# Optimization experiments

Hardware: AMD Instinct MI355X
Metric: run time of the kernel (lower is better)

The kernel has to match this reference:

```python
import jax, jax.numpy as jnp
import numpy as np

DIM = 256
HEADS = 8
HEAD_DIM = DIM // HEADS
EPS = 1e-5


def layer_norm(x, g, b):
    mu = jnp.mean(x, axis=-1, keepdims=True)
    var = jnp.mean(jnp.square(x - mu), axis=-1, keepdims=True)
    return (x - mu) * jax.lax.rsqrt(var + EPS) * g + b


def setup_inputs() -> dict:
    key = jax.random.key(0)
    ks = jax.random.split(key, 10)
    s = 0.02
    return {
        "x": jax.random.normal(ks[0], (4, DIM, 64, 64), dtype=jnp.float32),
        "g1": jnp.ones((DIM,), jnp.float32),
        "b1": jnp.zeros((DIM,), jnp.float32),
        "Wqkv": jax.random.normal(ks[1], (DIM, 3 * DIM), jnp.float32) * s,
        "Wp": jax.random.normal(ks[2], (DIM, DIM), jnp.float32) * s,
        "bp": jnp.zeros((DIM,), jnp.float32),
        "g2": jnp.ones((DIM,), jnp.float32),
        "b2": jnp.zeros((DIM,), jnp.float32),
        "W1": jax.random.normal(ks[3], (DIM, 2 * DIM), jnp.float32) * s,
        "bf1": jnp.zeros((2 * DIM,), jnp.float32),
        "W2": jax.random.normal(ks[4], (2 * DIM, DIM), jnp.float32) * s,
        "bf2": jnp.zeros((DIM,), jnp.float32),
    }


def reference(x, g1, b1, Wqkv, Wp, bp, g2, b2, W1, bf1, W2, bf2):
    B, C, H, W = x.shape
    N = H * W
    scale = HEAD_DIM ** -0.5
    tokens = x.reshape(B, C, N).transpose(0, 2, 1)  # [B,N,C]
    t = layer_norm(tokens, g1, b1)
    qkv = (t @ Wqkv).reshape(B, N, 3, HEADS, HEAD_DIM)
    q = qkv[:, :, 0].transpose(0, 2, 1, 3)  # [B,h,N,d]
    k = qkv[:, :, 1].transpose(0, 2, 1, 3)
    v = qkv[:, :, 2].transpose(0, 2, 1, 3)
    attn = jax.nn.softmax(jnp.einsum("bhnd,bhmd->bhnm", q, k) * scale, axis=-1)
    out = jnp.einsum("bhnm,bhmd->bhnd", attn, v)
    out = out.transpose(0, 2, 1, 3).reshape(B, N, C)
    tokens = tokens + out @ Wp + bp
    t2 = layer_norm(tokens, g2, b2)
    h = jax.nn.gelu(t2 @ W1 + bf1, approximate=False)
    tokens = tokens + h @ W2 + bf2
    return tokens.transpose(0, 2, 1).reshape(B, C, H, W)
```

## Files before the change

### kernel.cpp

```cpp
#include <hip/hip_runtime.h>

typedef unsigned short u16;
typedef unsigned int   u32;

using bf16x8 = __attribute__((ext_vector_type(8))) __bf16;
using f32x4  = __attribute__((ext_vector_type(4))) float;
using f32x16 = __attribute__((ext_vector_type(16))) float;

#define MFMA16(a, b, c) __builtin_amdgcn_mfma_f32_16x16x32_bf16((a), (b), (c), 0, 0, 0)
#define MFMA32(a, b, c) __builtin_amdgcn_mfma_f32_32x32x16_bf16((a), (b), (c), 0, 0, 0)

__device__ inline u16 f2bf(float f) {
  u32 x = __float_as_uint(f);
  return (u16)((x + 0x7FFFu + ((x >> 16) & 1u)) >> 16);
}

__device__ inline const bf16x8* bfp(const u16* p) {
  return reinterpret_cast<const bf16x8*>(p);
}

__global__ __launch_bounds__(256) void k_conv(
    const float* __restrict__ Wqkv, const float* __restrict__ Wp,
    const float* __restrict__ W1,   const float* __restrict__ W2,
    u16* __restrict__ wqkvT, u16* __restrict__ wpT,
    u16* __restrict__ w1T,   u16* __restrict__ w2T) {
  __shared__ float tile[32][33];
  int blk = blockIdx.x;
  const float* src; u16* dst; int R, C, t;
  if (blk < 192)      { src = Wqkv; dst = wqkvT; R = 256; C = 768; t = blk; }
  else if (blk < 256) { src = Wp;   dst = wpT;   R = 256; C = 256; t = blk - 192; }
  else if (blk < 384) { src = W1;   dst = w1T;   R = 256; C = 512; t = blk - 256; }
  else                { src = W2;   dst = w2T;   R = 512; C = 256; t = blk - 384; }
  int tpc = C >> 5;
  int tr = (t / tpc) << 5, tc = (t % tpc) << 5;
  int j = threadIdx.x & 31, iq = threadIdx.x >> 5;
  #pragma unroll
  for (int i = 0; i < 4; ++i)
    tile[iq + 8 * i][j] = src[(size_t)(tr + iq + 8 * i) * C + tc + j];
  __syncthreads();
  #pragma unroll
  for (int i = 0; i < 4; ++i)
    dst[(size_t)(tc + iq + 8 * i) * R + tr + j] = f2bf(tile[j][iq + 8 * i]);
}

__global__ __launch_bounds__(256) void k_ln1(
    const float* __restrict__ x, const float* __restrict__ g1,
    const float* __restrict__ b1, float* __restrict__ tokens,
    u16* __restrict__ ln) {
  __shared__ float tile[256][33];
  __shared__ float red[2][8][32];
  __shared__ float stat[2][32];
  int tid = threadIdx.x;
  int blk = blockIdx.x;
  int b = blk >> 7, n0 = (blk & 127) << 5;
  {
    int cq = tid >> 5, j = tid & 31;
    const float* xp = x + (((size_t)b * 256) << 12) + n0 + j;
    #pragma unroll 8
    for (int it = 0; it < 32; ++it) {
      int c = it * 8 + cq;
      tile[c][j] = xp[(size_t)c << 12];
    }
  }
  __syncthreads();
  {
    int tn = tid & 31, qq = tid >> 5;
    float s = 0.f, s2 = 0.f;
    #pragma unroll 8
    for (int i = 0; i < 32; ++i) {
      float v = tile[qq * 32 + i][tn];
      s += v; s2 += v * v;
    }
    red[0][qq][tn] = s; red[1][qq][tn] = s2;
  }
  __syncthreads();
  if (tid < 32) {
    float su = 0.f, sq = 0.f;
    #pragma unroll
    for (int qq = 0; qq < 8; ++qq) { su += red[0][qq][tid]; sq += red[1][qq][tid]; }
    float mu  = su * (1.f / 256.f);
    float var = sq * (1.f / 256.f) - mu * mu;
    stat[0][tid] = mu;
    stat[1][tid] = rsqrtf(var + 1e-5f);
  }
  __syncthreads();
  float g = g1[tid], bb = b1[tid];
  size_t base = ((size_t)(b * 4096 + n0)) * 256 + tid;
  for (int it = 0; it < 32; ++it) {
    float v = tile[tid][it];
    float y = (v - stat[0][it]) * stat[1][it] * g + bb;
    tokens[base + (size_t)it * 256] = v;
    ln[base + (size_t)it * 256] = f2bf(y);
  }
}

template <int K>
__device__ inline void mm16(const u16* __restrict__ A, const u16* __restrict__ BT,
                            int arow, int bcol, f32x4 acc[4]) {
  int lane = threadIdx.x & 63;
  int r = lane & 15, g = lane >> 4;
  const u16* ap  = A  + (size_t)(arow + r) * K + g * 8;
  const u16* bp0 = BT + (size_t)(bcol + r) * K + g * 8;
  #pragma unroll 4
  for (int k0 = 0; k0 < K; k0 += 32) {
    bf16x8 a = *bfp(ap + k0);
    #pragma unroll
    for (int nt = 0; nt < 4; ++nt) {
      bf16x8 b = *bfp(bp0 + nt * 16 * K + k0);
      acc[nt] = MFMA16(a, b, acc[nt]);
    }
  }
}

template <int K>
__device__ inline void mm32(const u16* __restrict__ A, const u16* __restrict__ BT,
                            int arow, int bcol, f32x4 acc[2][4]) {
  int lane = threadIdx.x & 63;
  int r = lane & 15, g = lane >> 4;
  const u16* ap0 = A  + (size_t)(arow + r) * K + g * 8;
  const u16* bp0 = BT + (size_t)(bcol + r) * K + g * 8;
  #pragma unroll 4
  for (int k0 = 0; k0 < K; k0 += 32) {
    bf16x8 a0 = *bfp(ap0 + k0);
    bf16x8 a1 = *bfp(ap0 + 16 * K + k0);
    #pragma unroll
    for (int nt = 0; nt < 4; ++nt) {
      bf16x8 b = *bfp(bp0 + nt * 16 * K + k0);
      acc[0][nt] = MFMA16(a0, b, acc[0][nt]);
      acc[1][nt] = MFMA16(a1, b, acc[1][nt]);
    }
  }
}

__global__ __launch_bounds__(256) void k_qkv(
    const u16* __restrict__ ln, const u16* __restrict__ wT,
    u16* __restrict__ q, u16* __restrict__ kf, u16* __restrict__ vf) {
  int w = threadIdx.x >> 6, lane = threadIdx.x & 63;
  int r16 = lane & 15, g4 = lane >> 4;
  int m0 = blockIdx.y * 128 + w * 32;
  int n0 = blockIdx.x * 64;
  f32x4 z = {0.f, 0.f, 0.f, 0.f};
  f32x4 acc[2][4] = {{z, z, z, z}, {z, z, z, z}};
  mm32<256>(ln, wT, m0, n0, acc);
  int b = m0 >> 12;
  const float qs = (float)(0.17677669529663687 * 1.4426950408889634);
  #pragma unroll
  for (int rg = 0; rg < 2; ++rg) {
    int nbase = (m0 & 4095) + rg * 16 + g4 * 4;
    #pragma unroll
    for (int nt = 0; nt < 4; ++nt) {
      int col = n0 + nt * 16 + r16;
      int which = col >> 8, h = (col >> 5) & 7, d = col & 31;
      size_t bh_off = ((size_t)(b * 8 + h)) << 17;
      if (which == 0) {
        #pragma unroll
        for (int r = 0; r < 4; ++r)
          q[((size_t)(b * 8 + h) * 4096 + nbase + r) * 32 + d] =
              f2bf(acc[rg][nt][r] * qs);
      } else if (which == 1) {
        int sel = d >> 4, lh = (d >> 3) & 1, jj = d & 7;
        #pragma unroll
        for (int r = 0; r < 4; ++r) {
          int key = nbase + r;
          kf[bh_off + (size_t)(key >> 5) * 1024 + sel * 512 +
             (((key & 31) | (lh << 5)) << 3) + jj] = f2bf(acc[rg][nt][r]);
        }
      } else {
        int kk = nbase & 31;
        int sel = kk >> 4, lh = (kk >> 3) & 1, j0 = kk & 7;
        ushort4 o4;
        o4.x = f2bf(acc[rg][nt][0]); o4.y = f2bf(acc[rg][nt][1]);
        o4.z = f2bf(acc[rg][nt][2]); o4.w = f2bf(acc[rg][nt][3]);
        *(ushort4*)(vf + bh_off + (size_t)(nbase >> 5) * 1024 + sel * 512 +
                    ((d | (lh << 5)) << 3) + j0) = o4;
      }
    }
  }
}

__global__ __launch_bounds__(512) void k_attn(
    const u16* __restrict__ q, const u16* __restrict__ kf,
    const u16* __restrict__ vf, u16* __restrict__ attnout) {
  __shared__ float obuf[4][64][17];
  __shared__ float lsbuf[4][64];
  int lane = threadIdx.x & 63;
  int w = threadIdx.x >> 6;
  int qi = w >> 1, kj = w & 1;
  int r32 = lane & 31, hi = lane >> 5;
  int bh = blockIdx.x >> 5;
  int qt = blockIdx.x & 31;
  int q0 = qt * 128 + qi * 32;
  const u16* qh = q + ((size_t)bh << 17);
  bf16x8 qf0 = *bfp(qh + (size_t)(q0 + r32) * 32 + hi * 8);
  bf16x8 qf1 = *bfp(qh + (size_t)(q0 + r32) * 32 + 16 + hi * 8);

  const u16* kp = kf + ((size_t)bh << 17) + (size_t)kj * 65536 + lane * 8;
  const u16* vp = vf + ((size_t)bh << 17) + (size_t)kj * 65536 + lane * 8;

  f32x16 o, zz;
  #pragma unroll
  for (int r = 0; r < 16; ++r) { o[r] = 0.f; zz[r] = 0.f; }
  float lsum = 0.f;

  bf16x8 ka0 = *bfp(kp);
  bf16x8 ka1 = *bfp(kp + 512);
  bf16x8 va0 = *bfp(vp);
  bf16x8 va1 = *bfp(vp + 512);
  kp += 1024; vp += 1024;

  #pragma unroll 2
  for (int c = 0; c < 64; ++c) {
    bf16x8 kb0 = *bfp(kp);
    bf16x8 kb1 = *bfp(kp + 512);
    bf16x8 vb0 = *bfp(vp);
    bf16x8 vb1 = *bfp(vp + 512);
    kp += 1024; vp += 1024;

    f32x16 s = MFMA32(ka0, qf0, zz);
    s = MFMA32(ka1, qf1, s);
    #pragma unroll
    for (int r = 0; r < 16; ++r) s[r] = __builtin_amdgcn_exp2f(s[r]);
    float t0 = ((s[0] + s[1]) + (s[2] + s[3])) + ((s[4] + s[5]) + (s[6] + s[7]));
    float t1 = ((s[8] + s[9]) + (s[10] + s[11])) + ((s[12] + s[13]) + (s[14] + s[15]));
    lsum += t0 + t1;
    u32 c8[8];
    #pragma unroll
    for (int i = 0; i < 8; ++i)
      asm("v_cvt_pk_bf16_f32 %0, %1, %2" : "=v"(c8[i]) : "v"(s[2 * i]), "v"(s[2 * i + 1]));
    asm("v_permlane32_swap_b32 %0, %1" : "+v"(c8[0]), "+v"(c8[2]));
    asm("v_permlane32_swap_b32 %0, %1" : "+v"(c8[1]), "+v"(c8[3]));
    asm("v_permlane32_swap_b32 %0, %1" : "+v"(c8[4]), "+v"(c8[6]));
    asm("v_permlane32_swap_b32 %0, %1" : "+v"(c8[5]), "+v"(c8[7]));
    union { u32 u[4]; bf16x8 v; } pf0, pf1;
    pf0.u[0] = c8[0]; pf0.u[1] = c8[1]; pf0.u[2] = c8[2]; pf0.u[3] = c8[3];
    pf1.u[0] = c8[4]; pf1.u[1] = c8[5]; pf1.u[2] = c8[6]; pf1.u[3] = c8[7];
    o = MFMA32(va0, pf0.v, o);
    o = MFMA32(va1, pf1.v, o);

    ka0 = kb0; ka1 = kb1; va0 = vb0; va1 = vb1;
  }

  lsum += __shfl_xor(lsum, 32);

  if (kj == 1) {
    #pragma unroll
    for (int g = 0; g < 16; ++g) obuf[qi][lane][g] = o[g];
    lsbuf[qi][lane] = lsum;
  }
  __syncthreads();
  if (kj == 0) {
    float inv = __builtin_amdgcn_rcpf(lsum + lsbuf[qi][lane]);
    int b = bh >> 3, h = bh & 7;
    size_t nrow = ((size_t)(b * 4096 + q0 + r32)) * 256 + h * 32;
    #pragma unroll
    for (int g = 0; g < 4; ++g) {
      ushort4 ov;
      ov.x = f2bf((o[g * 4 + 0] + obuf[qi][lane][g * 4 + 0]) * inv);
      ov.y = f2bf((o[g * 4 + 1] + obuf[qi][lane][g * 4 + 1]) * inv);
      ov.z = f2bf((o[g * 4 + 2] + obuf[qi][lane][g * 4 + 2]) * inv);
      ov.w = f2bf((o[g * 4 + 3] + obuf[qi][lane][g * 4 + 3]) * inv);
      *(ushort4*)(attnout + nrow + g * 8 + hi * 4) = ov;
    }
  }
}

__global__ __launch_bounds__(256) void k_projln(
    const u16* __restrict__ ao, const u16* __restrict__ wT,
    const float* __restrict__ bp, const float* __restrict__ g2,
    const float* __restrict__ b2, float* __restrict__ tokens,
    u16* __restrict__ ln) {
  __shared__ float red[2][4][16];
  int w = threadIdx.x >> 6, lane = threadIdx.x & 63;
  int r16 = lane & 15, g4 = lane >> 4;
  int m0 = blockIdx.x * 16;
  int n0 = w * 64;
  f32x4 z = {0.f, 0.f, 0.f, 0.f};
  f32x4 acc[4] = {z, z, z, z};
  mm16<256>(ao, wT, m0, n0, acc);
  float sum[4] = {0.f, 0.f, 0.f, 0.f}, sq[4] = {0.f, 0.f, 0.f, 0.f};
  #pragma unroll
  for (int nt = 0; nt < 4; ++nt) {
    int col = n0 + nt * 16 + r16;
    float bias = bp[col];
    #pragma unroll
    for (int r = 0; r < 4; ++r) {
      float v = tokens[(size_t)(m0 + g4 * 4 + r) * 256 + col] + acc[nt][r] + bias;
      acc[nt][r] = v;
      sum[r] += v; sq[r] += v * v;
    }
  }
  #pragma unroll
  for (int mask = 1; mask < 16; mask <<= 1) {
    #pragma unroll
    for (int r = 0; r < 4; ++r) {
      sum[r] += __shfl_xor(sum[r], mask);
      sq[r]  += __shfl_xor(sq[r], mask);
    }
  }
  if (r16 == 0) {
    #pragma unroll
    for (int r = 0; r < 4; ++r) {
      red[0][w][g4 * 4 + r] = sum[r];
      red[1][w][g4 * 4 + r] = sq[r];
    }
  }
  __syncthreads();
  float mu[4], rs[4];
  #pragma unroll
  for (int r = 0; r < 4; ++r) {
    int ri = g4 * 4 + r;
    float S  = red[0][0][ri] + red[0][1][ri] + red[0][2][ri] + red[0][3][ri];
    float SQ = red[1][0][ri] + red[1][1][ri] + red[1][2][ri] + red[1][3][ri];
    mu[r] = S * (1.f / 256.f);
    rs[r] = rsqrtf(SQ * (1.f / 256.f) - mu[r] * mu[r] + 1e-5f);
  }
  #pragma unroll
  for (int nt = 0; nt < 4; ++nt) {
    int col = n0 + nt * 16 + r16;
    float gg = g2[col], bb = b2[col];
    #pragma unroll
    for (int r = 0; r < 4; ++r) {
      size_t idx = (size_t)(m0 + g4 * 4 + r) * 256 + col;
      float v = acc[nt][r];
      tokens[idx] = v;
      ln[idx] = f2bf((v - mu[r]) * rs[r] * gg + bb);
    }
  }
}

__global__ __launch_bounds__(512) void k_mlp(
    const u16* __restrict__ ln, const u16* __restrict__ w1T,
    const float* __restrict__ bf1, const u16* __restrict__ w2T,
    const float* __restrict__ bf2, const float* __restrict__ tokens,
    float* __restrict__ out) {
  __shared__ u16 hh[32][520];
  int w = threadIdx.x >> 6, lane = threadIdx.x & 63;
  int r16 = lane & 15, g4 = lane >> 4;
  int rh = w & 1, cg = w >> 1;
  int m0 = blockIdx.x * 32 + rh * 16;
  {
    f32x4 z = {0.f, 0.f, 0.f, 0.f};
    f32x4 acc[8] = {z, z, z, z, z, z, z, z};
    const u16* ap  = ln  + (size_t)(m0 + r16) * 256 + g4 * 8;
    const u16* bp0 = w1T + (size_t)(cg * 128 + r16) * 256 + g4 * 8;
    #pragma unroll 2
    for (int k0 = 0; k0 < 256; k0 += 32) {
      bf16x8 a = *bfp(ap + k0);
      #pragma unroll
      for (int nt = 0; nt < 8; ++nt) {
        bf16x8 b = *bfp(bp0 + nt * 16 * 256 + k0);
        acc[nt] = MFMA16(a, b, acc[nt]);
      }
    }
    int rl = rh * 16 + g4 * 4;
    #pragma unroll
    for (int nt = 0; nt < 8; ++nt) {
      int col = cg * 128 + nt * 16 + r16;
      float bias = bf1[col];
      #pragma unroll
      for (int r = 0; r < 4; ++r) {
        float xx = acc[nt][r] + bias;
        float x2 = xx * xx;
        float zt = xx * (2.3021188f + 0.10293855f * x2);
        float e  = __builtin_amdgcn_exp2f(zt);
        float ge = xx * (1.f - __builtin_amdgcn_rcpf(1.f + e));
        hh[rl + r][col] = f2bf(ge);
      }
    }
  }
  __syncthreads();
  f32x4 z = {0.f, 0.f, 0.f, 0.f};
  f32x4 acc[4] = {z, z, z, z};
  const u16* hrow = &hh[rh * 16 + r16][g4 * 8];
  const u16* bp2  = w2T + (size_t)(cg * 64 + r16) * 512 + g4 * 8;
  #pragma unroll 4
  for (int k0 = 0; k0 < 512; k0 += 32) {
    bf16x8 a = *bfp(hrow + k0);
    #pragma unroll
    for (int nt = 0; nt < 4; ++nt) {
      bf16x8 b = *bfp(bp2 + nt * 16 * 512 + k0);
      acc[nt] = MFMA16(a, b, acc[nt]);
    }
  }
  int b = m0 >> 12;
  int nl = (m0 & 4095) + g4 * 4;
  #pragma unroll
  for (int nt = 0; nt < 4; ++nt) {
    int col = cg * 64 + nt * 16 + r16;
    float bias = bf2[col];
    float4 o;
    o.x = tokens[(size_t)(m0 + g4 * 4 + 0) * 256 + col] + acc[nt][0] + bias;
    o.y = tokens[(size_t)(m0 + g4 * 4 + 1) * 256 + col] + acc[nt][1] + bias;
    o.z = tokens[(size_t)(m0 + g4 * 4 + 2) * 256 + col] + acc[nt][2] + bias;
    o.w = tokens[(size_t)(m0 + g4 * 4 + 3) * 256 + col] + acc[nt][3] + bias;
    *(float4*)(out + (((size_t)(b * 256 + col)) << 12) + nl) = o;
  }
}

extern "C" void kernel_launch(void* const* d_in, const int* in_sizes, int n_in,
                              void* d_out, int out_size, void* d_ws, size_t ws_size,
                              hipStream_t stream) {
  (void)in_sizes; (void)n_in; (void)out_size; (void)ws_size;
  const float* x    = (const float*)d_in[0];
  const float* g1   = (const float*)d_in[1];
  const float* b1   = (const float*)d_in[2];
  const float* Wqkv = (const float*)d_in[3];
  const float* Wp   = (const float*)d_in[4];
  const float* bp   = (const float*)d_in[5];
  const float* g2   = (const float*)d_in[6];
  const float* b2   = (const float*)d_in[7];
  const float* W1   = (const float*)d_in[8];
  const float* bf1  = (const float*)d_in[9];
  const float* W2   = (const float*)d_in[10];
  const float* bf2  = (const float*)d_in[11];
  float* out = (float*)d_out;

  char* ws = (char*)d_ws;
  float* tokens = (float*)(ws);
  u16* lnb      = (u16*)(ws + 16777216);
  u16* qb       = (u16*)(ws + 25165824);
  u16* kfb      = (u16*)(ws + 33554432);
  u16* vfb      = (u16*)(ws + 41943040);
  u16* aob      = (u16*)(ws + 50331648);
  u16* wqkvT    = (u16*)(ws + 67108864);
  u16* wpT      = (u16*)(ws + 67502080);
  u16* w1T      = (u16*)(ws + 67633152);
  u16* w2T      = (u16*)(ws + 67895296);

  k_conv  <<<512, 256, 0, stream>>>(Wqkv, Wp, W1, W2, wqkvT, wpT, w1T, w2T);
  k_ln1   <<<512, 256, 0, stream>>>(x, g1, b1, tokens, lnb);
  k_qkv   <<<dim3(12, 128), 256, 0, stream>>>(lnb, wqkvT, qb, kfb, vfb);
  k_attn  <<<1024, 512, 0, stream>>>(qb, kfb, vfb, aob);
  k_projln<<<1024, 256, 0, stream>>>(aob, wpT, bp, g2, b2, tokens, lnb);
  k_mlp   <<<512, 512, 0, stream>>>(lnb, w1T, bf1, w2T, bf2, tokens, out);
}
```

Measured before the change: 239.6 us.

## Process two query tiles per wave in attention to reuse K/V fragments

Each attention wave now handles 64 queries (two 32-row tiles) instead of 32, so every K/V fragment loaded from global memory feeds two sets of score and PV MFMAs. The grid is halved to 512 blocks, and the software prefetch of the next K/V chunk is dropped, with loads issued at the top of each iteration instead. Launch bounds now request 4 waves per SIMD. The cost is roughly double the accumulator registers and LDS per block, and fewer blocks to spread across CUs.

```diff
diff --git a/kernel.cpp b/kernel.cpp
--- a/kernel.cpp
+++ b/kernel.cpp
@@ -178,88 +178,119 @@
   }
 }
 
-__global__ __launch_bounds__(512) void k_attn(
+__global__ __launch_bounds__(512, 4) void k_attn(
     const u16* __restrict__ q, const u16* __restrict__ kf,
     const u16* __restrict__ vf, u16* __restrict__ attnout) {
-  __shared__ float obuf[4][64][17];
-  __shared__ float lsbuf[4][64];
+  __shared__ float obuf[4][2][64][17];
+  __shared__ float lsbuf[4][2][64];
   int lane = threadIdx.x & 63;
   int w = threadIdx.x >> 6;
   int qi = w >> 1, kj = w & 1;
   int r32 = lane & 31, hi = lane >> 5;
-  int bh = blockIdx.x >> 5;
-  int qt = blockIdx.x & 31;
-  int q0 = qt * 128 + qi * 32;
+  int bh = blockIdx.x >> 4;
+  int qt = blockIdx.x & 15;
+  int q0 = qt * 256 + qi * 64;
   const u16* qh = q + ((size_t)bh << 17);
-  bf16x8 qf0 = *bfp(qh + (size_t)(q0 + r32) * 32 + hi * 8);
-  bf16x8 qf1 = *bfp(qh + (size_t)(q0 + r32) * 32 + 16 + hi * 8);
+  bf16x8 qf00 = *bfp(qh + (size_t)(q0 + r32) * 32 + hi * 8);
+  bf16x8 qf01 = *bfp(qh + (size_t)(q0 + r32) * 32 + 16 + hi * 8);
+  bf16x8 qf10 = *bfp(qh + (size_t)(q0 + 32 + r32) * 32 + hi * 8);
+  bf16x8 qf11 = *bfp(qh + (size_t)(q0 + 32 + r32) * 32 + 16 + hi * 8);
 
   const u16* kp = kf + ((size_t)bh << 17) + (size_t)kj * 65536 + lane * 8;
   const u16* vp = vf + ((size_t)bh << 17) + (size_t)kj * 65536 + lane * 8;
 
-  f32x16 o, zz;
-  #pragma unroll
-  for (int r = 0; r < 16; ++r) { o[r] = 0.f; zz[r] = 0.f; }
-  float lsum = 0.f;
-
-  bf16x8 ka0 = *bfp(kp);
-  bf16x8 ka1 = *bfp(kp + 512);
-  bf16x8 va0 = *bfp(vp);
-  bf16x8 va1 = *bfp(vp + 512);
-  kp += 1024; vp += 1024;
+  f32x16 o0, o1, zz;
+  #pragma unroll
+  for (int r = 0; r < 16; ++r) { o0[r] = 0.f; o1[r] = 0.f; zz[r] = 0.f; }
+  float ls0 = 0.f, ls1 = 0.f;
 
   #pragma unroll 2
   for (int c = 0; c < 64; ++c) {
-    bf16x8 kb0 = *bfp(kp);
-    bf16x8 kb1 = *bfp(kp + 512);
-    bf16x8 vb0 = *bfp(vp);
-    bf16x8 vb1 = *bfp(vp + 512);
+    bf16x8 ka0 = *bfp(kp);
+    bf16x8 ka1 = *bfp(kp + 512);
+    bf16x8 va0 = *bfp(vp);
+    bf16x8 va1 = *bfp(vp + 512);
     kp += 1024; vp += 1024;
 
-    f32x16 s = MFMA32(ka0, qf0, zz);
-    s = MFMA32(ka1, qf1, s);
-    #pragma unroll
-    for (int r = 0; r < 16; ++r) s[r] = __builtin_amdgcn_exp2f(s[r]);
-    float t0 = ((s[0] + s[1]) + (s[2] + s[3])) + ((s[4] + s[5]) + (s[6] + s[7]));
-    float t1 = ((s[8] + s[9]) + (s[10] + s[11])) + ((s[12] + s[13]) + (s[14] + s[15]));
-    lsum += t0 + t1;
-    u32 c8[8];
-    #pragma unroll
-    for (int i = 0; i < 8; ++i)
-      asm("v_cvt_pk_bf16_f32 %0, %1, %2" : "=v"(c8[i]) : "v"(s[2 * i]), "v"(s[2 * i + 1]));
-    asm("v_permlane32_swap_b32 %0, %1" : "+v"(c8[0]), "+v"(c8[2]));
-    asm("v_permlane32_swap_b32 %0, %1" : "+v"(c8[1]), "+v"(c8[3]));
-    asm("v_permlane32_swap_b32 %0, %1" : "+v"(c8[4]), "+v"(c8[6]));
-    asm("v_permlane32_swap_b32 %0, %1" : "+v"(c8[5]), "+v"(c8[7]));
-    union { u32 u[4]; bf16x8 v; } pf0, pf1;
-    pf0.u[0] = c8[0]; pf0.u[1] = c8[1]; pf0.u[2] = c8[2]; pf0.u[3] = c8[3];
-    pf1.u[0] = c8[4]; pf1.u[1] = c8[5]; pf1.u[2] = c8[6]; pf1.u[3] = c8[7];
-    o = MFMA32(va0, pf0.v, o);
-    o = MFMA32(va1, pf1.v, o);
-
-    ka0 = kb0; ka1 = kb1; va0 = vb0; va1 = vb1;
-  }
-
-  lsum += __shfl_xor(lsum, 32);
+    {
+      f32x16 s = MFMA32(ka0, qf00, zz);
+      s = MFMA32(ka1, qf01, s);
+      #pragma unroll
+      for (int r = 0; r < 16; ++r) s[r] = __builtin_amdgcn_exp2f(s[r]);
+      float t0 = ((s[0] + s[1]) + (s[2] + s[3])) + ((s[4] + s[5]) + (s[6] + s[7]));
+      float t1 = ((s[8] + s[9]) + (s[10] + s[11])) + ((s[12] + s[13]) + (s[14] + s[15]));
+      ls0 += t0 + t1;
+      u32 c8[8];
+      #pragma unroll
+      for (int i = 0; i < 8; ++i)
+        asm("v_cvt_pk_bf16_f32 %0, %1, %2" : "=v"(c8[i]) : "v"(s[2 * i]), "v"(s[2 * i + 1]));
+      asm("v_permlane32_swap_b32 %0, %1" : "+v"(c8[0]), "+v"(c8[2]));
+      asm("v_permlane32_swap_b32 %0, %1" : "+v"(c8[1]), "+v"(c8[3]));
+      asm("v_permlane32_swap_b32 %0, %1" : "+v"(c8[4]), "+v"(c8[6]));
+      asm("v_permlane32_swap_b32 %0, %1" : "+v"(c8[5]), "+v"(c8[7]));
+      union { u32 u[4]; bf16x8 v; } pf0, pf1;
+      pf0.u[0] = c8[0]; pf0.u[1] = c8[1]; pf0.u[2] = c8[2]; pf0.u[3] = c8[3];
+      pf1.u[0] = c8[4]; pf1.u[1] = c8[5]; pf1.u[2] = c8[6]; pf1.u[3] = c8[7];
+      o0 = MFMA32(va0, pf0.v, o0);
+      o0 = MFMA32(va1, pf1.v, o0);
+    }
+    {
+      f32x16 s = MFMA32(ka0, qf10, zz);
+      s = MFMA32(ka1, qf11, s);
+      #pragma unroll
+      for (int r = 0; r < 16; ++r) s[r] = __builtin_amdgcn_exp2f(s[r]);
+      float t0 = ((s[0] + s[1]) + (s[2] + s[3])) + ((s[4] + s[5]) + (s[6] + s[7]));
+      float t1 = ((s[8] + s[9]) + (s[10] + s[11])) + ((s[12] + s[13]) + (s[14] + s[15]));
+      ls1 += t0 + t1;
+      u32 c8[8];
+      #pragma unroll
+      for (int i = 0; i < 8; ++i)
+        asm("v_cvt_pk_bf16_f32 %0, %1, %2" : "=v"(c8[i]) : "v"(s[2 * i]), "v"(s[2 * i + 1]));
+      asm("v_permlane32_swap_b32 %0, %1" : "+v"(c8[0]), "+v"(c8[2]));
+      asm("v_permlane32_swap_b32 %0, %1" : "+v"(c8[1]), "+v"(c8[3]));
+      asm("v_permlane32_swap_b32 %0, %1" : "+v"(c8[4]), "+v"(c8[6]));
+      asm("v_permlane32_swap_b32 %0, %1" : "+v"(c8[5]), "+v"(c8[7]));
+      union { u32 u[4]; bf16x8 v; } pf0, pf1;
+      pf0.u[0] = c8[0]; pf0.u[1] = c8[1]; pf0.u[2] = c8[2]; pf0.u[3] = c8[3];
+      pf1.u[0] = c8[4]; pf1.u[1] = c8[5]; pf1.u[2] = c8[6]; pf1.u[3] = c8[7];
+      o1 = MFMA32(va0, pf0.v, o1);
+      o1 = MFMA32(va1, pf1.v, o1);
+    }
+  }
+
+  ls0 += __shfl_xor(ls0, 32);
+  ls1 += __shfl_xor(ls1, 32);
 
   if (kj == 1) {
     #pragma unroll
-    for (int g = 0; g < 16; ++g) obuf[qi][lane][g] = o[g];
-    lsbuf[qi][lane] = lsum;
+    for (int g = 0; g < 16; ++g) {
+      obuf[qi][0][lane][g] = o0[g];
+      obuf[qi][1][lane][g] = o1[g];
+    }
+    lsbuf[qi][0][lane] = ls0;
+    lsbuf[qi][1][lane] = ls1;
   }
   __syncthreads();
   if (kj == 0) {
-    float inv = __builtin_amdgcn_rcpf(lsum + lsbuf[qi][lane]);
     int b = bh >> 3, h = bh & 7;
-    size_t nrow = ((size_t)(b * 4096 + q0 + r32)) * 256 + h * 32;
+    float inv0 = __builtin_amdgcn_rcpf(ls0 + lsbuf[qi][0][lane]);
+    float inv1 = __builtin_amdgcn_rcpf(ls1 + lsbuf[qi][1][lane]);
+    size_t nrow0 = ((size_t)(b * 4096 + q0 + r32)) * 256 + h * 32;
+    size_t nrow1 = ((size_t)(b * 4096 + q0 + 32 + r32)) * 256 + h * 32;
     #pragma unroll
     for (int g = 0; g < 4; ++g) {
       ushort4 ov;
-      ov.x = f2bf((o[g * 4 + 0] + obuf[qi][lane][g * 4 + 0]) * inv);
-      ov.y = f2bf((o[g * 4 + 1] + obuf[qi][lane][g * 4 + 1]) * inv);
-      ov.z = f2bf((o[g * 4 + 2] + obuf[qi][lane][g * 4 + 2]) * inv);
-      ov.w = f2bf((o[g * 4 + 3] + obuf[qi][lane][g * 4 + 3]) * inv);
-      *(ushort4*)(attnout + nrow + g * 8 + hi * 4) = ov;
+      ov.x = f2bf((o0[g * 4 + 0] + obuf[qi][0][lane][g * 4 + 0]) * inv0);
+      ov.y = f2bf((o0[g * 4 + 1] + obuf[qi][0][lane][g * 4 + 1]) * inv0);
+      ov.z = f2bf((o0[g * 4 + 2] + obuf[qi][0][lane][g * 4 + 2]) * inv0);
+      ov.w = f2bf((o0[g * 4 + 3] + obuf[qi][0][lane][g * 4 + 3]) * inv0);
+      *(ushort4*)(attnout + nrow0 + g * 8 + hi * 4) = ov;
+      ushort4 ow;
+      ow.x = f2bf((o1[g * 4 + 0] + obuf[qi][1][lane][g * 4 + 0]) * inv1);
+      ow.y = f2bf((o1[g * 4 + 1] + obuf[qi][1][lane][g * 4 + 1]) * inv1);
+      ow.z = f2bf((o1[g * 4 + 2] + obuf[qi][1][lane][g * 4 + 2]) * inv1);
+      ow.w = f2bf((o1[g * 4 + 3] + obuf[qi][1][lane][g * 4 + 3]) * inv1);
+      *(ushort4*)(attnout + nrow1 + g * 8 + hi * 4) = ow;
     }
   }
 }
@@ -430,7 +461,7 @@
   k_conv  <<<512, 256, 0, stream>>>(Wqkv, Wp, W1, W2, wqkvT, wpT, w1T, w2T);
   k_ln1   <<<512, 256, 0, stream>>>(x, g1, b1, tokens, lnb);
   k_qkv   <<<dim3(12, 128), 256, 0, stream>>>(lnb, wqkvT, qb, kfb, vfb);
-  k_attn  <<<1024, 512, 0, stream>>>(qb, kfb, vfb, aob);
+  k_attn  <<<512, 512, 0, stream>>>(qb, kfb, vfb, aob);
   k_projln<<<1024, 256, 0, stream>>>(aob, wpT, bp, g2, b2, tokens, lnb);
   k_mlp   <<<512, 512, 0, stream>>>(lnb, w1T, bf1, w2T, bf2, tokens, out);
 }
```

New measurement: 233.4 us. -2.6%, faster.
